# Kernel optimization log

Measured on AMD Instinct MI355X. Metric: run time of the kernel, lower is better.

The kernel has to match this reference:

```python
import jax, jax.numpy as jnp
import numpy as np

B, NE, NMAX = 256, 90, 270
ZE = PE = GE = PPS = 32
NPROPS = 20
FP, SGE, LATH = 256, 64, 128
PIN = FP + SGE + LATH  # 448 = pred_inp_size = conv input (add_to_node)
C1, C2, H = 448, 256, 3
P1 = P2 = 512
EPS = 1e-5

PNAMES = ['sg_emb_table','lat_W1','lat_b1','lat_bn1_g','lat_bn1_b','lat_bn1_m','lat_bn1_v',
          'lat_W2','lat_b2','lat_bn2_g','lat_bn2_b','lat_bn2_m','lat_bn2_v',
          'z_emb_table','period_table','group_table','props','W_props','b_props','W_phys','b_phys',
          'gat1_W','gat1_as','gat1_ad','gat1_b','gat2_W','gat2_as','gat2_ad','gat2_b',
          'pW1','pb1','pbn1_g','pbn1_b','pbn1_m','pbn1_v',
          'pW2','pb2','pbn2_g','pbn2_b','pbn2_m','pbn2_v','pW3','pb3']

def _bn(x, g, b, m, v):
    return (x - m) * g / jnp.sqrt(v + EPS) + b

def _lrelu(x, s=0.2):
    return jnp.where(x >= 0, x, s * x)

def _gat(x, adj, W, a_s, a_d, bias):
    # PyG DenseGATConv: concat=False (mean over heads), dropout=0, negative_slope=0.2
    Bn, N, _ = x.shape
    h = (x @ W).reshape(Bn, N, H, -1)                      # [B,N,H,C]
    asrc = (h * a_s).sum(-1)                               # [B,N,H]
    adst = (h * a_d).sum(-1)
    alpha = asrc[:, None, :, :] + adst[:, :, None, :]      # [B,i,j,H]
    alpha = _lrelu(alpha, 0.2)
    adj_sl = jnp.maximum(adj, jnp.eye(N, dtype=adj.dtype))  # add self loops
    alpha = jnp.where(adj_sl[..., None] > 0, alpha, -jnp.inf)
    alpha = jax.nn.softmax(alpha, axis=2)                  # softmax over sources j
    out = jnp.einsum('bijh,bjhc->bihc', alpha, h)
    return out.mean(2) + bias                              # [B,N,C]

def _forward(comp, sg, lat, period_idx, group_idx, p):
    sg_x = p['sg_emb_table'][sg[:, 0]]                     # [B,SGE]
    # lattice MLP: (Linear -> BN -> LeakyReLU(True)==identity) x2
    h = _bn(lat @ p['lat_W1'] + p['lat_b1'], p['lat_bn1_g'], p['lat_bn1_b'], p['lat_bn1_m'], p['lat_bn1_v'])
    lat_x = _bn(h @ p['lat_W2'] + p['lat_b2'], p['lat_bn2_g'], p['lat_bn2_b'], p['lat_bn2_m'], p['lat_bn2_v'])
    # ragged -> dense batch: expand composition counts into dense node-type grid
    n_atoms = comp.sum(1)                                  # [B]
    cum = jnp.cumsum(comp, axis=1)                         # [B,NE]
    t = jnp.arange(NMAX)
    z = jax.vmap(lambda c: jnp.searchsorted(c, t, side='right'))(cum)  # [B,NMAX]
    mask = t[None, :] < n_atoms[:, None]                   # [B,NMAX] valid nodes
    z = jnp.where(mask, z, 0)
    # PhysEmbedding: z/period/group embeddings + projected properties -> final proj
    phys = jnp.concatenate([
        p['z_emb_table'][z],
        p['period_table'][period_idx[z]],
        p['group_table'][group_idx[z]],
        p['props'][z] @ p['W_props'] + p['b_props'],
    ], axis=-1)
    phys = phys @ p['W_phys'] + p['b_phys']                # [B,NMAX,FP]
    # add_to_node: cat graph-level lat/sg embeddings onto every node, then zero-pad
    node = jnp.concatenate([
        phys,
        jnp.broadcast_to(lat_x[:, None, :], (lat_x.shape[0], NMAX, LATH)),
        jnp.broadcast_to(sg_x[:, None, :], (sg_x.shape[0], NMAX, SGE)),
    ], axis=-1)
    node = node * mask[..., None].astype(node.dtype)       # to_dense_batch zero padding
    # per-graph dense block adjacency, zero diagonal (fill_diagonal_(0))
    adj = (mask[:, :, None] & mask[:, None, :]).astype(node.dtype)
    adj = adj * (1.0 - jnp.eye(NMAX, dtype=node.dtype))
    # GNNBlock: act = LeakyReLU(True) == identity (negative_slope=1)
    x1 = _gat(node, adj, p['gat1_W'], p['gat1_as'], p['gat1_ad'], p['gat1_b'])
    x2 = _gat(x1, adj, p['gat2_W'], p['gat2_as'], p['gat2_ad'], p['gat2_b'])
    comp_x = x2.sum(1)                                     # sum over ALL NMAX slots (incl. padding, as torch does)
    feat = jnp.concatenate([comp_x, sg_x, lat_x], axis=-1) # [B,PIN]
    # prediction head (eval: dropout off, BN running stats)
    h = _lrelu(_bn(feat @ p['pW1'] + p['pb1'], p['pbn1_g'], p['pbn1_b'], p['pbn1_m'], p['pbn1_v']))
    h = _lrelu(_bn(h @ p['pW2'] + p['pb2'], p['pbn2_g'], p['pbn2_b'], p['pbn2_m'], p['pbn2_v']))
    return h @ p['pW3'] + p['pb3']                         # [B,1]

def setup_inputs():
    key = jax.random.key(0)
    ks = iter(jax.random.split(key, 64))
    def nrm(shape, s=0.05):
        return jax.random.normal(next(ks), shape, dtype=jnp.float32) * s
    comp = jax.random.randint(next(ks), (B, NE), 0, 4, dtype=jnp.int32)
    comp = comp.at[0].set(3)  # graph 0 has exactly NMAX atoms -> data N_max == NMAX
    sg = jax.random.randint(next(ks), (B, 1), 0, 230)
    lat = jax.random.uniform(next(ks), (B, 6), dtype=jnp.float32)
    period_idx = jax.random.randint(next(ks), (NE,), 0, 8)
    group_idx = jax.random.randint(next(ks), (NE,), 0, 19)
    inp = dict(comp=comp, sg=sg, lat=lat, period_idx=period_idx, group_idx=group_idx)
    inp.update(
        sg_emb_table=nrm((230, SGE)),
        lat_W1=nrm((6, LATH)), lat_b1=nrm((LATH,)),
        lat_bn1_g=jnp.ones(LATH), lat_bn1_b=jnp.zeros(LATH), lat_bn1_m=jnp.zeros(LATH), lat_bn1_v=jnp.ones(LATH),
        lat_W2=nrm((LATH, LATH)), lat_b2=nrm((LATH,)),
        lat_bn2_g=jnp.ones(LATH), lat_bn2_b=jnp.zeros(LATH), lat_bn2_m=jnp.zeros(LATH), lat_bn2_v=jnp.ones(LATH),
        z_emb_table=nrm((NE, ZE)), period_table=nrm((8, PE)), group_table=nrm((19, GE)),
        props=nrm((NE, NPROPS), 0.1), W_props=nrm((NPROPS, PPS)), b_props=nrm((PPS,)),
        W_phys=nrm((ZE + PE + GE + PPS, FP)), b_phys=nrm((FP,)),
        gat1_W=nrm((PIN, H * C1)), gat1_as=nrm((H, C1)), gat1_ad=nrm((H, C1)), gat1_b=nrm((C1,)),
        gat2_W=nrm((C1, H * C2)), gat2_as=nrm((H, C2)), gat2_ad=nrm((H, C2)), gat2_b=nrm((C2,)),
        pW1=nrm((PIN, P1)), pb1=nrm((P1,)),
        pbn1_g=jnp.ones(P1), pbn1_b=jnp.zeros(P1), pbn1_m=jnp.zeros(P1), pbn1_v=jnp.ones(P1),
        pW2=nrm((P1, P2)), pb2=nrm((P2,)),
        pbn2_g=jnp.ones(P2), pbn2_b=jnp.zeros(P2), pbn2_m=jnp.zeros(P2), pbn2_v=jnp.ones(P2),
        pW3=nrm((P2, 1)), pb3=nrm((1,)),
    )
    return inp

def reference(comp, sg, lat, period_idx, group_idx,
              sg_emb_table, lat_W1, lat_b1, lat_bn1_g, lat_bn1_b, lat_bn1_m, lat_bn1_v,
              lat_W2, lat_b2, lat_bn2_g, lat_bn2_b, lat_bn2_m, lat_bn2_v,
              z_emb_table, period_table, group_table, props, W_props, b_props, W_phys, b_phys,
              gat1_W, gat1_as, gat1_ad, gat1_b, gat2_W, gat2_as, gat2_ad, gat2_b,
              pW1, pb1, pbn1_g, pbn1_b, pbn1_m, pbn1_v,
              pW2, pb2, pbn2_g, pbn2_b, pbn2_m, pbn2_v, pW3, pb3):
    vals = (sg_emb_table, lat_W1, lat_b1, lat_bn1_g, lat_bn1_b, lat_bn1_m, lat_bn1_v,
            lat_W2, lat_b2, lat_bn2_g, lat_bn2_b, lat_bn2_m, lat_bn2_v,
            z_emb_table, period_table, group_table, props, W_props, b_props, W_phys, b_phys,
            gat1_W, gat1_as, gat1_ad, gat1_b, gat2_W, gat2_as, gat2_ad, gat2_b,
            pW1, pb1, pbn1_g, pbn1_b, pbn1_m, pbn1_v,
            pW2, pb2, pbn2_g, pbn2_b, pbn2_m, pbn2_v, pW3, pb3)
    p = dict(zip(PNAMES, vals))
    return _forward(comp, sg, lat, period_idx, group_idx, p)
```

## Files before the change

### kernel.cpp

```cpp
#include <hip/hip_runtime.h>
#include <math.h>

#define BB 256
#define NEL 90
#define NMAX 270
#define C1 448
#define C2 256
#define PIN 448
#define LATH 128
#define SGE 64
#define P1 512
#define EPSB 1e-5f

typedef short shortx8 __attribute__((ext_vector_type(8)));
typedef float floatx4 __attribute__((ext_vector_type(4)));

__device__ __forceinline__ float bf2f(unsigned short u) {
  return __uint_as_float(((unsigned)u) << 16);
}
__device__ __forceinline__ unsigned short f2bf(float f) {
  unsigned x = __float_as_uint(f);
  unsigned r = (x + 0x7fffu + ((x >> 16) & 1u)) >> 16;
  return (unsigned short)r;
}

#define NB_PREP  BB
#define NB_SCAN  1
#define NB_PHYS  NEL
#define NB_WP1   (14 * 42)
#define NB_WP2   (14 * 24)
#define NB_FOLD  112
#define NB_PAD   64
#define SETUP_GRID (NB_PREP + NB_SCAN + NB_PHYS + NB_WP1 + NB_WP2 + 2 * NB_FOLD + NB_PAD)

__global__ __launch_bounds__(256) void k_setup(
    const int* __restrict__ comp, const int* __restrict__ sg, const float* __restrict__ lat,
    const float* __restrict__ sg_emb,
    const float* __restrict__ lW1, const float* __restrict__ lb1,
    const float* __restrict__ lg1, const float* __restrict__ lbe1,
    const float* __restrict__ lm1, const float* __restrict__ lv1,
    const float* __restrict__ lW2, const float* __restrict__ lb2,
    const float* __restrict__ lg2, const float* __restrict__ lbe2,
    const float* __restrict__ lm2, const float* __restrict__ lv2,
    const int* __restrict__ period_idx, const int* __restrict__ group_idx,
    const float* __restrict__ z_emb, const float* __restrict__ period_t,
    const float* __restrict__ group_t, const float* __restrict__ props,
    const float* __restrict__ Wp, const float* __restrict__ bp,
    const float* __restrict__ Wphys, const float* __restrict__ bphys,
    const float* __restrict__ gat1_W, const float* __restrict__ gat1_as,
    const float* __restrict__ gat1_ad, const float* __restrict__ gat1_b,
    const float* __restrict__ gat2_W, const float* __restrict__ gat2_as,
    const float* __restrict__ gat2_ad, const float* __restrict__ gat2_b,
    float* __restrict__ sgx, float* __restrict__ latx, int* __restrict__ z,
    int* __restrict__ natoms, int* __restrict__ off, int* __restrict__ aoff,
    float* __restrict__ zerobuf, float* __restrict__ physpe,
    unsigned short* __restrict__ wt1, unsigned short* __restrict__ wt2,
    float* __restrict__ wsv1, float* __restrict__ wdv1,
    float* __restrict__ wsv2, float* __restrict__ wdv2, float* __restrict__ pad2) {
  int r = blockIdx.x;
  int tid = threadIdx.x;
  int wv = tid >> 6, lane = tid & 63;

  if (r < NB_PREP) {
    int b = r;
    __shared__ int cum[NEL];
    __shared__ float hbuf[LATH];
    __shared__ float latl[6];
    if (tid == 0) {
      int s = 0;
      for (int e = 0; e < NEL; ++e) { s += comp[b * NEL + e]; cum[e] = s; }
    }
    if (tid < 6) latl[tid] = lat[b * 6 + tid];
    __syncthreads();
    int n = cum[NEL - 1];
    for (int t = tid; t < NMAX; t += 256) {
      int zz = -1;
      if (t < n) {
        for (int e = 0; e < NEL; ++e) { if (cum[e] > t) { zz = e; break; } }
      }
      z[b * NMAX + t] = zz;
    }
    if (tid < SGE) sgx[b * SGE + tid] = sg_emb[sg[b] * SGE + tid];
    if (tid < LATH) {
      float acc = lb1[tid];
      for (int k = 0; k < 6; ++k) acc += latl[k] * lW1[k * LATH + tid];
      acc = (acc - lm1[tid]) * lg1[tid] * rsqrtf(lv1[tid] + EPSB) + lbe1[tid];
      hbuf[tid] = acc;
    }
    __syncthreads();
    if (tid < LATH) {
      float acc = lb2[tid];
      for (int k = 0; k < LATH; ++k) acc += hbuf[k] * lW2[k * LATH + tid];
      acc = (acc - lm2[tid]) * lg2[tid] * rsqrtf(lv2[tid] + EPSB) + lbe2[tid];
      latx[b * LATH + tid] = acc;
    }
    return;
  }
  r -= NB_PREP;
  if (r < NB_SCAN) {
    __shared__ int sh[BB];
    zerobuf[tid] = 0.f;
    int v0 = 0;
    for (int e = 0; e < NEL; ++e) v0 += comp[tid * NEL + e];
    natoms[tid] = v0;
    sh[tid] = v0;
    for (int d = 1; d < BB; d <<= 1) {
      __syncthreads();
      int v = (tid >= d) ? sh[tid - d] : 0;
      __syncthreads();
      sh[tid] += v;
    }
    __syncthreads();
    off[tid] = sh[tid] - v0;
    __syncthreads();
    int sz = 3 * ((((v0 + 15) >> 4) << 4)) * ((((v0 + 31) >> 5) << 5));
    sh[tid] = sz;
    for (int d = 1; d < BB; d <<= 1) {
      __syncthreads();
      int v = (tid >= d) ? sh[tid - d] : 0;
      __syncthreads();
      sh[tid] += v;
    }
    __syncthreads();
    aoff[tid] = sh[tid] - sz;
    return;
  }
  r -= NB_SCAN;
  if (r < NB_PHYS) {
    int e = r;
    __shared__ float ph[128];
    if (tid < 32) ph[tid] = z_emb[e * 32 + tid];
    else if (tid < 64) ph[tid] = period_t[period_idx[e] * 32 + tid - 32];
    else if (tid < 96) ph[tid] = group_t[group_idx[e] * 32 + tid - 64];
    else if (tid < 128) {
      int j = tid - 96;
      float acc = bp[j];
      for (int k = 0; k < 20; ++k) acc += props[e * 20 + k] * Wp[k * 32 + j];
      ph[tid] = acc;
    }
    __syncthreads();
    float acc = bphys[tid];
    for (int k = 0; k < 128; ++k) acc += ph[k] * Wphys[k * 256 + tid];
    physpe[e * 256 + tid] = acc;
    return;
  }
  r -= NB_PHYS;
  if (r < NB_WP1 + NB_WP2) {
    const float* W;
    unsigned short* Wt;
    int NC3, bx, by;
    if (r < NB_WP1) { W = gat1_W; Wt = wt1; NC3 = 3 * C1; bx = r % 14; by = r / 14; }
    else { int r2 = r - NB_WP1; W = gat2_W; Wt = wt2; NC3 = 3 * C2; bx = r2 % 14; by = r2 / 14; }
    int k0 = bx << 5, c0 = by << 5;
    __shared__ float ts[32][33];
    int e4 = tid << 2;
    int kk = e4 >> 5, cc = e4 & 31;
    float4 v = *(const float4*)(W + (size_t)(k0 + kk) * NC3 + c0 + cc);
    ts[kk][cc] = v.x; ts[kk][cc + 1] = v.y; ts[kk][cc + 2] = v.z; ts[kk][cc + 3] = v.w;
    __syncthreads();
    int c2 = tid & 31, kg = tid >> 5;
    ushort4 u;
    u.x = f2bf(ts[kg * 4 + 0][c2]); u.y = f2bf(ts[kg * 4 + 1][c2]);
    u.z = f2bf(ts[kg * 4 + 2][c2]); u.w = f2bf(ts[kg * 4 + 3][c2]);
    *(ushort4*)(Wt + (size_t)(c0 + c2) * 448 + k0 + (kg << 2)) = u;
    return;
  }
  r -= NB_WP1 + NB_WP2;
  if (r < 2 * NB_FOLD) {
    const float* W; const float* as_; const float* ad_;
    float* wsv; float* wdv; int NC3, C, kb;
    if (r < NB_FOLD) { W = gat1_W; as_ = gat1_as; ad_ = gat1_ad; wsv = wsv1; wdv = wdv1; NC3 = 3 * C1; C = C1; kb = r << 2; }
    else { int r2 = r - NB_FOLD; W = gat2_W; as_ = gat2_as; ad_ = gat2_ad; wsv = wsv2; wdv = wdv2; NC3 = 3 * C2; C = C2; kb = r2 << 2; }
    int k = kb + wv;
    for (int h = 0; h < 3; ++h) {
      float ss = 0.f, sd = 0.f;
      for (int c = lane; c < C; c += 64) {
        float wvv = W[(size_t)k * NC3 + h * C + c];
        ss += wvv * as_[h * C + c];
        sd += wvv * ad_[h * C + c];
      }
      for (int o = 32; o > 0; o >>= 1) { ss += __shfl_xor(ss, o); sd += __shfl_xor(sd, o); }
      if (lane == 0) { wsv[k * 3 + h] = ss; wdv[k * 3 + h] = sd; }
    }
    return;
  }
  r -= 2 * NB_FOLD;
  {
    int c = (r << 2) + wv;
    float s = 0.f;
    for (int k = lane; k < C1; k += 64) {
      const float* wr = gat2_W + (size_t)k * (3 * C2) + c;
      s += gat1_b[k] * (wr[0] + wr[C2] + wr[2 * C2]);
    }
    for (int o = 32; o > 0; o >>= 1) s += __shfl_xor(s, o);
    if (lane == 0) pad2[c] = s * (1.f / 3.f) + gat2_b[c];
  }
}

__global__ __launch_bounds__(256) void k_nodep(
    const int* __restrict__ z, const int* __restrict__ off, const int* __restrict__ natoms,
    const float* __restrict__ physpe, const float* __restrict__ latx,
    const float* __restrict__ sgx, unsigned short* __restrict__ x0) {
  int b = blockIdx.x;
  int n = natoms[b], ob = off[b];
  int tid = threadIdx.x;
  __shared__ int zl[NMAX];
  for (int t = tid; t < n; t += 256) zl[t] = z[b * NMAX + t];
  __syncthreads();
  int items = n * 56;
  for (int e = tid; e < items; e += 256) {
    int t = e / 56, c8 = (e - t * 56) << 3;
    int zt = zl[t];
    float v[8];
    if (c8 < 256) {
      float4 a = *(const float4*)(physpe + zt * 256 + c8);
      float4 c = *(const float4*)(physpe + zt * 256 + c8 + 4);
      v[0] = a.x; v[1] = a.y; v[2] = a.z; v[3] = a.w;
      v[4] = c.x; v[5] = c.y; v[6] = c.z; v[7] = c.w;
    } else if (c8 < 384) {
      float4 a = *(const float4*)(latx + b * LATH + c8 - 256);
      float4 c = *(const float4*)(latx + b * LATH + c8 - 252);
      v[0] = a.x; v[1] = a.y; v[2] = a.z; v[3] = a.w;
      v[4] = c.x; v[5] = c.y; v[6] = c.z; v[7] = c.w;
    } else {
      float4 a = *(const float4*)(sgx + b * SGE + c8 - 384);
      float4 c = *(const float4*)(sgx + b * SGE + c8 - 380);
      v[0] = a.x; v[1] = a.y; v[2] = a.z; v[3] = a.w;
      v[4] = c.x; v[5] = c.y; v[6] = c.z; v[7] = c.w;
    }
    unsigned short u[8];
    #pragma unroll
    for (int i = 0; i < 8; ++i) u[i] = f2bf(v[i]);
    *(uint4*)(x0 + (size_t)(ob + t) * PIN + c8) = *(uint4*)u;
  }
}

__global__ __launch_bounds__(256) void k_av2(
    const unsigned short* __restrict__ x, const float* __restrict__ wsv,
    const float* __restrict__ wdv, const int* __restrict__ off,
    const int* __restrict__ natoms, float* __restrict__ asrc,
    float* __restrict__ adst, int K) {
  __shared__ float sw[C1 * 3], dw[C1 * 3];
  int tid = threadIdx.x;
  for (int e = tid; e < K * 3; e += 256) { sw[e] = wsv[e]; dw[e] = wdv[e]; }
  __syncthreads();
  int total = off[BB - 1] + natoms[BB - 1];
  int wv = tid >> 6, lane = tid & 63;
  int nk8 = K >> 3;
  int stride = gridDim.x << 2;
  for (int row = (blockIdx.x << 2) + wv; row < total; row += stride) {
    float s0 = 0.f, s1 = 0.f, s2 = 0.f, d0 = 0.f, d1 = 0.f, d2 = 0.f;
    if (lane < nk8) {
      uint4 raw = *(const uint4*)(x + (size_t)row * K + (lane << 3));
      unsigned short us[8];
      *(uint4*)us = raw;
      #pragma unroll
      for (int u = 0; u < 8; ++u) {
        float xv = bf2f(us[u]);
        int kb = ((lane << 3) + u) * 3;
        s0 += xv * sw[kb + 0]; s1 += xv * sw[kb + 1]; s2 += xv * sw[kb + 2];
        d0 += xv * dw[kb + 0]; d1 += xv * dw[kb + 1]; d2 += xv * dw[kb + 2];
      }
    }
    #pragma unroll
    for (int o = 32; o > 0; o >>= 1) {
      s0 += __shfl_xor(s0, o); s1 += __shfl_xor(s1, o); s2 += __shfl_xor(s2, o);
      d0 += __shfl_xor(d0, o); d1 += __shfl_xor(d1, o); d2 += __shfl_xor(d2, o);
    }
    if (lane == 0) {
      asrc[row * 3 + 0] = s0; asrc[row * 3 + 1] = s1; asrc[row * 3 + 2] = s2;
      adst[row * 3 + 0] = d0; adst[row * 3 + 1] = d1; adst[row * 3 + 2] = d2;
    }
  }
}

#define MTMAX 17
__global__ __launch_bounds__(256) void k_alpha(
    const float* __restrict__ asrc, const float* __restrict__ adst,
    const int* __restrict__ off, const int* __restrict__ natoms,
    const int* __restrict__ aoff, unsigned short* __restrict__ alpha) {
  int bid = blockIdx.x;
  int b = bid & (BB - 1);
  int hm = bid >> 8;
  int h = hm % 3;
  int mt = hm / 3;
  int n = natoms[b];
  if (n == 0) return;
  int mtn = (n + 15) >> 4;
  if (mt >= mtn) return;
  int ktn = (n + 31) >> 5;
  int rext = mtn << 4, kext = ktn << 5;
  int ob = off[b];
  size_t ab = (size_t)aoff[b] + (size_t)h * rext * kext;
  int tid = threadIdx.x;
  int wv = tid >> 6, lane = tid & 63;
  __shared__ float asl[288];
  for (int j = tid; j < kext; j += 256)
    asl[j] = (j < n) ? asrc[(ob + j) * 3 + h] : 0.f;
  __syncthreads();
  #pragma unroll
  for (int r = 0; r < 4; ++r) {
    int i = (mt << 4) + (wv << 2) + r;
    unsigned short* rowp = alpha + ab + (size_t)i * kext;
    if (i >= n) {
      for (int j = lane; j < kext; j += 64) rowp[j] = 0;
      continue;
    }
    float ad = adst[(ob + i) * 3 + h];
    float m = -1e30f;
    for (int j = lane; j < n; j += 64) {
      float sc = asl[j] + ad;
      sc = fmaxf(sc, 0.2f * sc);
      m = fmaxf(m, sc);
    }
    for (int o = 32; o > 0; o >>= 1) m = fmaxf(m, __shfl_xor(m, o));
    float s = 0.f;
    for (int j = lane; j < n; j += 64) {
      float sc = asl[j] + ad;
      sc = fmaxf(sc, 0.2f * sc);
      s += __expf(sc - m);
    }
    for (int o = 32; o > 0; o >>= 1) s += __shfl_xor(s, o);
    float rs = 1.f / s;
    for (int j = lane; j < kext; j += 64) {
      float v = 0.f;
      if (j < n) {
        float sc = asl[j] + ad;
        sc = fmaxf(sc, 0.2f * sc);
        v = __expf(sc - m) * rs;
      }
      rowp[j] = f2bf(v);
    }
  }
}

#define MTW 5

__global__ __launch_bounds__(256, 2) void k_fused_mfma(
    const unsigned short* __restrict__ xin, const unsigned short* __restrict__ Wt,
    const unsigned short* __restrict__ alpha, const int* __restrict__ aoff,
    const int* __restrict__ off, const int* __restrict__ natoms,
    const float* __restrict__ bias, const float* __restrict__ zerobuf,
    unsigned short* __restrict__ xout, int K, int C, int NC) {
  int bid = blockIdx.x;
  int xg = bid & 7;
  int g = bid >> 3;
  int cblk = g % NC;
  int b = xg + ((g / NC) << 3);
  int c0 = cblk << 6;
  int n = natoms[b];
  if (n == 0) return;
  int ob = off[b];
  size_t ab = (size_t)aoff[b];
  int tid = threadIdx.x;
  int wv = tid >> 6;
  int lane = tid & 63;
  int m16 = lane & 15;
  int q = lane >> 4;

  int mtn = (n + 15) >> 4;
  int jmax = mtn << 4;
  int ktn = (n + 31) >> 5;
  int kext = ktn << 5;
  size_t hstride = (size_t)jmax * kext;

  __shared__ unsigned short tt[36 * 512];

  const unsigned short* xsrc[MTW];
  #pragma unroll
  for (int t_i = 0; t_i < MTW; ++t_i) {
    int mt = wv + (t_i << 2);
    int j = (mt << 4) + m16;
    xsrc[t_i] = (j < n) ? (xin + (size_t)(ob + j) * 448 + (q << 3))
                        : (const unsigned short*)zerobuf;
  }

  floatx4 acc[MTW][4];
  #pragma unroll
  for (int i = 0; i < MTW; ++i)
    #pragma unroll
    for (int nt = 0; nt < 4; ++nt) acc[i][nt] = (floatx4)0.f;

  for (int h = 0; h < 3; ++h) {
    floatx4 tac[MTW][4];
    #pragma unroll
    for (int i = 0; i < MTW; ++i)
      #pragma unroll
      for (int nt = 0; nt < 4; ++nt) tac[i][nt] = (floatx4)0.f;

    const unsigned short* wbase = Wt + (size_t)(h * C + c0 + m16) * 448 + (q << 3);

    #pragma unroll 2
    for (int k0 = 0; k0 < 448; k0 += 32) {
      shortx8 bfr[4];
      #pragma unroll
      for (int nt = 0; nt < 4; ++nt)
        bfr[nt] = *(const shortx8*)(wbase + (size_t)(nt << 4) * 448 + k0);
      #pragma unroll
      for (int t_i = 0; t_i < MTW; ++t_i) {
        int mt = wv + (t_i << 2);
        if (mt < mtn) {
          shortx8 a = *(const shortx8*)(xsrc[t_i] + k0);
          #pragma unroll
          for (int nt = 0; nt < 4; ++nt)
            tac[t_i][nt] = __builtin_amdgcn_mfma_f32_16x16x32_bf16(a, bfr[nt], tac[t_i][nt], 0, 0, 0);
        }
      }
    }

    #pragma unroll
    for (int t_i = 0; t_i < MTW; ++t_i) {
      int mt = wv + (t_i << 2);
      if (mt < mtn) {
        int jbase = (mt << 4) + (q << 2);
        #pragma unroll
        for (int nt = 0; nt < 4; ++nt) {
          floatx4 d = tac[t_i][nt];
          ushort4 u;
          u.x = f2bf(d.x); u.y = f2bf(d.y); u.z = f2bf(d.z); u.w = f2bf(d.w);
          int c = (nt << 4) + m16;
          *(ushort4*)(tt + ((jbase >> 3) << 9) + (c << 3) + (jbase & 7)) = u;
        }
      }
    }
    for (int e = tid; e < ((kext - jmax) << 6); e += 256) {
      int j = jmax + (e >> 6), c = e & 63;
      tt[((j >> 3) << 9) + (c << 3) + (j & 7)] = 0;
    }
    __syncthreads();
    const unsigned short* ap = alpha + ab + (size_t)h * hstride;
    for (int k0p = 0; k0p < kext; k0p += 32) {
      shortx8 tb[4];
      #pragma unroll
      for (int nt = 0; nt < 4; ++nt)
        tb[nt] = *(const shortx8*)(tt + (((k0p >> 3) + q) << 9) + (((nt << 4) + m16) << 3));
      #pragma unroll
      for (int t_i = 0; t_i < MTW; ++t_i) {
        int mt = wv + (t_i << 2);
        if (mt < mtn) {
          shortx8 af = *(const shortx8*)(ap + (size_t)((mt << 4) + m16) * kext + k0p + (q << 3));
          #pragma unroll
          for (int nt = 0; nt < 4; ++nt)
            acc[t_i][nt] = __builtin_amdgcn_mfma_f32_16x16x32_bf16(af, tb[nt], acc[t_i][nt], 0, 0, 0);
        }
      }
    }
    __syncthreads();
  }
  float bq[4];
  #pragma unroll
  for (int nt = 0; nt < 4; ++nt) bq[nt] = bias[c0 + (nt << 4) + m16];
  const float inv3 = 1.f / 3.f;
  #pragma unroll
  for (int t_i = 0; t_i < MTW; ++t_i) {
    int mt = wv + (t_i << 2);
    if (mt < mtn) {
      #pragma unroll
      for (int nt = 0; nt < 4; ++nt) {
        floatx4 d = acc[t_i][nt];
        int cidx = c0 + (nt << 4) + m16;
        #pragma unroll
        for (int r = 0; r < 4; ++r) {
          int i = (mt << 4) + (q << 2) + r;
          if (i < n) xout[(size_t)(ob + i) * C + cidx] = f2bf(d[r] * inv3 + bq[nt]);
        }
      }
    }
  }
}

__global__ __launch_bounds__(512) void k_feat_head(
    const unsigned short* __restrict__ x2, const float* __restrict__ pad2,
    const int* __restrict__ off, const int* __restrict__ natoms,
    const float* __restrict__ sgx, const float* __restrict__ latx,
    const float* __restrict__ W1, const float* __restrict__ b1,
    const float* __restrict__ g1, const float* __restrict__ be1,
    const float* __restrict__ m1, const float* __restrict__ v1,
    const float* __restrict__ W2, const float* __restrict__ b2,
    const float* __restrict__ g2, const float* __restrict__ be2,
    const float* __restrict__ m2, const float* __restrict__ v2,
    const float* __restrict__ W3, const float* __restrict__ b3,
    float* __restrict__ out) {
  int b = blockIdx.x, tid = threadIdx.x;
  int wv8 = tid >> 6, lane = tid & 63;
  int n = natoms[b], ob = off[b];
  __shared__ float part[8][256];
  __shared__ float f[PIN];
  __shared__ float h1[P1];
  __shared__ float h2[P1];
  __shared__ float red[512];
  float a0 = 0.f, a1 = 0.f, a2 = 0.f, a3 = 0.f;
  for (int r = wv8; r < n; r += 8) {
    uint2 raw = *(const uint2*)(x2 + (size_t)(ob + r) * C2 + (lane << 2));
    unsigned short us[4];
    *(uint2*)us = raw;
    a0 += bf2f(us[0]); a1 += bf2f(us[1]); a2 += bf2f(us[2]); a3 += bf2f(us[3]);
  }
  {
    float4 p = make_float4(a0, a1, a2, a3);
    *(float4*)&part[wv8][lane << 2] = p;
  }
  __syncthreads();
  if (tid < 256) {
    float s = 0.f;
    #pragma unroll
    for (int w = 0; w < 8; ++w) s += part[w][tid];
    f[tid] = s + (float)(NMAX - n) * pad2[tid];
  } else if (tid < 320) {
    f[tid] = sgx[b * SGE + (tid - 256)];
  } else if (tid < 448) {
    f[tid] = latx[b * LATH + (tid - 320)];
  }
  __syncthreads();
  {
    int o = tid;
    float acc = b1[o];
    for (int k = 0; k < PIN; ++k) acc += f[k] * W1[k * P1 + o];
    acc = (acc - m1[o]) * g1[o] * rsqrtf(v1[o] + EPSB) + be1[o];
    h1[o] = acc >= 0.f ? acc : 0.2f * acc;
  }
  __syncthreads();
  {
    int o = tid;
    float acc = b2[o];
    for (int k = 0; k < P1; ++k) acc += h1[k] * W2[k * P1 + o];
    acc = (acc - m2[o]) * g2[o] * rsqrtf(v2[o] + EPSB) + be2[o];
    h2[o] = acc >= 0.f ? acc : 0.2f * acc;
  }
  __syncthreads();
  red[tid] = h2[tid] * W3[tid];
  __syncthreads();
  for (int s = 256; s > 0; s >>= 1) {
    if (tid < s) red[tid] += red[tid + s];
    __syncthreads();
  }
  if (tid == 0) out[b] = red[0] + b3[0];
}

extern "C" void kernel_launch(void* const* d_in, const int* in_sizes, int n_in,
                              void* d_out, int out_size, void* d_ws, size_t ws_size,
                              hipStream_t stream) {
  const int*   comp       = (const int*)d_in[0];
  const int*   sg         = (const int*)d_in[1];
  const float* lat        = (const float*)d_in[2];
  const int*   period_idx = (const int*)d_in[3];
  const int*   group_idx  = (const int*)d_in[4];
  const float* sg_emb     = (const float*)d_in[5];
  const float* lat_W1     = (const float*)d_in[6];
  const float* lat_b1     = (const float*)d_in[7];
  const float* lat_bn1_g  = (const float*)d_in[8];
  const float* lat_bn1_b  = (const float*)d_in[9];
  const float* lat_bn1_m  = (const float*)d_in[10];
  const float* lat_bn1_v  = (const float*)d_in[11];
  const float* lat_W2     = (const float*)d_in[12];
  const float* lat_b2     = (const float*)d_in[13];
  const float* lat_bn2_g  = (const float*)d_in[14];
  const float* lat_bn2_b  = (const float*)d_in[15];
  const float* lat_bn2_m  = (const float*)d_in[16];
  const float* lat_bn2_v  = (const float*)d_in[17];
  const float* z_emb      = (const float*)d_in[18];
  const float* period_t   = (const float*)d_in[19];
  const float* group_t    = (const float*)d_in[20];
  const float* props      = (const float*)d_in[21];
  const float* W_props    = (const float*)d_in[22];
  const float* b_props    = (const float*)d_in[23];
  const float* W_phys     = (const float*)d_in[24];
  const float* b_phys     = (const float*)d_in[25];
  const float* gat1_W     = (const float*)d_in[26];
  const float* gat1_as    = (const float*)d_in[27];
  const float* gat1_ad    = (const float*)d_in[28];
  const float* gat1_b     = (const float*)d_in[29];
  const float* gat2_W     = (const float*)d_in[30];
  const float* gat2_as    = (const float*)d_in[31];
  const float* gat2_ad    = (const float*)d_in[32];
  const float* gat2_b     = (const float*)d_in[33];
  const float* pW1        = (const float*)d_in[34];
  const float* pb1        = (const float*)d_in[35];
  const float* pbn1_g     = (const float*)d_in[36];
  const float* pbn1_b     = (const float*)d_in[37];
  const float* pbn1_m     = (const float*)d_in[38];
  const float* pbn1_v     = (const float*)d_in[39];
  const float* pW2        = (const float*)d_in[40];
  const float* pb2        = (const float*)d_in[41];
  const float* pbn2_g     = (const float*)d_in[42];
  const float* pbn2_b     = (const float*)d_in[43];
  const float* pbn2_m     = (const float*)d_in[44];
  const float* pbn2_v     = (const float*)d_in[45];
  const float* pW3        = (const float*)d_in[46];
  const float* pb3        = (const float*)d_in[47];

  float* ws = (float*)d_ws;
  const size_t o_sgx  = 0;
  const size_t o_latx = o_sgx  + (size_t)BB * SGE;
  const size_t o_nat  = o_latx + (size_t)BB * LATH;
  const size_t o_off  = o_nat  + BB;
  const size_t o_aoff = o_off  + BB;
  const size_t o_z    = o_aoff + BB;
  const size_t o_phys = o_z    + (size_t)BB * NMAX;
  const size_t o_wsv1 = o_phys + (size_t)NEL * 256;
  const size_t o_wdv1 = o_wsv1 + (size_t)C1 * 3;
  const size_t o_wsv2 = o_wdv1 + (size_t)C1 * 3;
  const size_t o_wdv2 = o_wsv2 + (size_t)C1 * 3;
  const size_t o_asrc = o_wdv2 + (size_t)C1 * 3;
  const size_t o_adst = o_asrc + (size_t)BB * NMAX * 3;
  const size_t o_pad2 = o_adst + (size_t)BB * NMAX * 3;
  const size_t o_zero = o_pad2 + 256;
  const size_t o_wt1  = o_zero + 256;
  const size_t o_wt2  = o_wt1  + (size_t)(3 * C1) * PIN / 2;
  const size_t o_x0   = o_wt2  + (size_t)(3 * C2) * C1 / 2;
  const size_t o_x1   = o_x0   + (size_t)BB * NMAX * PIN / 2;
  const size_t o_alph = o_x1   + (size_t)BB * NMAX * PIN / 2;

  float* sgx    = ws + o_sgx;
  float* latx   = ws + o_latx;
  int*   natoms = (int*)(ws + o_nat);
  int*   off    = (int*)(ws + o_off);
  int*   aoff   = (int*)(ws + o_aoff);
  int*   z      = (int*)(ws + o_z);
  float* physpe = ws + o_phys;
  float* wsv1   = ws + o_wsv1;
  float* wdv1   = ws + o_wdv1;
  float* wsv2   = ws + o_wsv2;
  float* wdv2   = ws + o_wdv2;
  float* asrc   = ws + o_asrc;
  float* adst   = ws + o_adst;
  float* pad2   = ws + o_pad2;
  float* zerobuf = ws + o_zero;
  unsigned short* wt1   = (unsigned short*)(ws + o_wt1);
  unsigned short* wt2   = (unsigned short*)(ws + o_wt2);
  unsigned short* x0    = (unsigned short*)(ws + o_x0);
  unsigned short* x1    = (unsigned short*)(ws + o_x1);
  unsigned short* x2    = x0;
  unsigned short* alpha = (unsigned short*)(ws + o_alph);

  const int ALG = BB * 3 * MTMAX;

  k_setup<<<SETUP_GRID, 256, 0, stream>>>(
      comp, sg, lat, sg_emb,
      lat_W1, lat_b1, lat_bn1_g, lat_bn1_b, lat_bn1_m, lat_bn1_v,
      lat_W2, lat_b2, lat_bn2_g, lat_bn2_b, lat_bn2_m, lat_bn2_v,
      period_idx, group_idx, z_emb, period_t, group_t, props,
      W_props, b_props, W_phys, b_phys,
      gat1_W, gat1_as, gat1_ad, gat1_b,
      gat2_W, gat2_as, gat2_ad, gat2_b,
      sgx, latx, z, natoms, off, aoff, zerobuf, physpe,
      wt1, wt2, wsv1, wdv1, wsv2, wdv2, pad2);

  k_nodep<<<BB, 256, 0, stream>>>(z, off, natoms, physpe, latx, sgx, x0);

  k_av2<<<1024, 256, 0, stream>>>(x0, wsv1, wdv1, off, natoms, asrc, adst, PIN);
  k_alpha<<<ALG, 256, 0, stream>>>(asrc, adst, off, natoms, aoff, alpha);
  k_fused_mfma<<<(C1 / 64) * BB, 256, 0, stream>>>(x0, wt1, alpha, aoff,
      off, natoms, gat1_b, zerobuf, x1, PIN, C1, C1 / 64);

  k_av2<<<1024, 256, 0, stream>>>(x1, wsv2, wdv2, off, natoms, asrc, adst, C1);
  k_alpha<<<ALG, 256, 0, stream>>>(asrc, adst, off, natoms, aoff, alpha);
  k_fused_mfma<<<(C2 / 64) * BB, 256, 0, stream>>>(x1, wt2, alpha, aoff,
      off, natoms, gat2_b, zerobuf, x2, C1, C2, C2 / 64);

  k_feat_head<<<BB, 512, 0, stream>>>(x2, pad2, off, natoms, sgx, latx,
      pW1, pb1, pbn1_g, pbn1_b, pbn1_m, pbn1_v,
      pW2, pb2, pbn2_g, pbn2_b, pbn2_m, pbn2_v,
      pW3, pb3, (float*)d_out);
}
```

Baseline: 878.0 us.

## Stage weight tiles into LDS via global_load_lds with XOR swizzle

Instead of every wave loading the weight B-fragments straight from global memory, the kernel stages a 32-row by 448-column weight slice into shared memory (reusing the tt buffer) with asynchronous global_load_lds. Reads use an XOR swizzle to avoid bank conflicts. The goal is to stop four waves from redundantly fetching the same weights and to cut global load latency in the MFMA inner loop. The cost is two extra block barriers per half-slice per head and no overlap between the staging load and compute, since the loads are not double-buffered.

New measurement: 832.6 us. 1.05x faster.

```diff
diff --git a/kernel.cpp b/kernel.cpp
--- a/kernel.cpp
+++ b/kernel.cpp
@@ -22,6 +22,11 @@
   unsigned x = __float_as_uint(f);
   unsigned r = (x + 0x7fffu + ((x >> 16) & 1u)) >> 16;
   return (unsigned short)r;
+}
+__device__ __forceinline__ void gld16(const void* g, void* l) {
+  __builtin_amdgcn_global_load_lds(
+      (const __attribute__((address_space(1))) unsigned int*)g,
+      (__attribute__((address_space(3))) unsigned int*)l, 16, 0, 0);
 }
 
 #define NB_PREP  BB
@@ -335,6 +340,8 @@
 }
 
 #define MTW 5
+#define WROWS 32
+#define WCH 56
 
 __global__ __launch_bounds__(256, 2) void k_fused_mfma(
     const unsigned short* __restrict__ xin, const unsigned short* __restrict__ Wt,
@@ -365,6 +372,16 @@
   size_t hstride = (size_t)jmax * kext;
 
   __shared__ unsigned short tt[36 * 512];
+  unsigned short* wlds = tt;
+
+  int swz16[7];
+  #pragma unroll
+  for (int i = 0; i < 7; ++i) {
+    int d16 = (i << 8) + tid;
+    int row = d16 / WCH;
+    int ch = d16 - row * WCH;
+    swz16[i] = row * WCH + (ch ^ (row & 7));
+  }
 
   const unsigned short* xsrc[MTW];
   #pragma unroll
@@ -388,24 +405,35 @@
       #pragma unroll
       for (int nt = 0; nt < 4; ++nt) tac[i][nt] = (floatx4)0.f;
 
-    const unsigned short* wbase = Wt + (size_t)(h * C + c0 + m16) * 448 + (q << 3);
-
-    #pragma unroll 2
-    for (int k0 = 0; k0 < 448; k0 += 32) {
-      shortx8 bfr[4];
+    #pragma unroll
+    for (int r = 0; r < 2; ++r) {
+      const unsigned short* wsl = Wt + (size_t)(h * C + c0 + r * WROWS) * 448;
       #pragma unroll
-      for (int nt = 0; nt < 4; ++nt)
-        bfr[nt] = *(const shortx8*)(wbase + (size_t)(nt << 4) * 448 + k0);
-      #pragma unroll
-      for (int t_i = 0; t_i < MTW; ++t_i) {
-        int mt = wv + (t_i << 2);
-        if (mt < mtn) {
-          shortx8 a = *(const shortx8*)(xsrc[t_i] + k0);
-          #pragma unroll
-          for (int nt = 0; nt < 4; ++nt)
-            tac[t_i][nt] = __builtin_amdgcn_mfma_f32_16x16x32_bf16(a, bfr[nt], tac[t_i][nt], 0, 0, 0);
+      for (int i = 0; i < 7; ++i)
+        gld16(wsl + ((size_t)swz16[i] << 3), wlds + ((((i << 8) + (wv << 6))) << 3));
+      __syncthreads();
+      #pragma unroll 2
+      for (int k0 = 0; k0 < 448; k0 += 32) {
+        int kq = (k0 >> 3) + q;
+        shortx8 bfr[2];
+        #pragma unroll
+        for (int nt2 = 0; nt2 < 2; ++nt2) {
+          int row = (nt2 << 4) + m16;
+          bfr[nt2] = *(const shortx8*)(wlds + row * 448 + ((kq ^ (row & 7)) << 3));
         }
-      }
+        #pragma unroll
+        for (int t_i = 0; t_i < MTW; ++t_i) {
+          int mt = wv + (t_i << 2);
+          if (mt < mtn) {
+            shortx8 a = *(const shortx8*)(xsrc[t_i] + k0);
+            tac[t_i][(r << 1) + 0] = __builtin_amdgcn_mfma_f32_16x16x32_bf16(
+                a, bfr[0], tac[t_i][(r << 1) + 0], 0, 0, 0);
+            tac[t_i][(r << 1) + 1] = __builtin_amdgcn_mfma_f32_16x16x32_bf16(
+                a, bfr[1], tac[t_i][(r << 1) + 1], 0, 0, 0);
+          }
+        }
+      }
+      __syncthreads();
     }
 
     #pragma unroll
```

## Split fused GAT kernel into global X·W GEMM and per-graph aggregation

Applied to the files above, without the earlier changes.

Replaces the per-graph fused kernel, which recomputed X·W for each graph and head inside a block, with a batch-wide tiled bf16 MFMA GEMM. The GEMM uses 128x64 tiles, double-buffered global_load_lds and a swizzled LDS layout, and writes transposed XW to a scratch buffer. A second kernel then does the alpha·XW aggregation per graph from that buffer. Node offsets are padded to multiples of 32 with zeroed pad rows so the aggregation can read contiguous K-tiles. The work is chunked across column blocks to keep the scratch buffer small. This improves weight reuse and MFMA utilisation, but adds a global-memory round trip and more kernel launches.

Measured after the change: 1.008 ms. +14.8%, slower.

```diff
diff --git a/kernel.cpp b/kernel.cpp
--- a/kernel.cpp
+++ b/kernel.cpp
@@ -12,6 +12,9 @@
 #define P1 512
 #define EPSB 1e-5f
 
+#define XROWCAP 44032
+#define GJT (XROWCAP / 128)
+
 typedef short shortx8 __attribute__((ext_vector_type(8)));
 typedef float floatx4 __attribute__((ext_vector_type(4)));
 
@@ -22,6 +25,11 @@
   unsigned x = __float_as_uint(f);
   unsigned r = (x + 0x7fffu + ((x >> 16) & 1u)) >> 16;
   return (unsigned short)r;
+}
+__device__ __forceinline__ void gld16(const void* g, void* l) {
+  __builtin_amdgcn_global_load_lds(
+      (const __attribute__((address_space(1))) unsigned int*)g,
+      (__attribute__((address_space(3))) unsigned int*)l, 16, 0, 0);
 }
 
 #define NB_PREP  BB
@@ -53,6 +61,7 @@
     const float* __restrict__ gat2_ad, const float* __restrict__ gat2_b,
     float* __restrict__ sgx, float* __restrict__ latx, int* __restrict__ z,
     int* __restrict__ natoms, int* __restrict__ off, int* __restrict__ aoff,
+    int* __restrict__ meta,
     float* __restrict__ zerobuf, float* __restrict__ physpe,
     unsigned short* __restrict__ wt1, unsigned short* __restrict__ wt2,
     float* __restrict__ wsv1, float* __restrict__ wdv1,
@@ -103,7 +112,8 @@
     int v0 = 0;
     for (int e = 0; e < NEL; ++e) v0 += comp[tid * NEL + e];
     natoms[tid] = v0;
-    sh[tid] = v0;
+    int kx = ((v0 + 31) >> 5) << 5;
+    sh[tid] = kx;
     for (int d = 1; d < BB; d <<= 1) {
       __syncthreads();
       int v = (tid >= d) ? sh[tid - d] : 0;
@@ -111,7 +121,8 @@
       sh[tid] += v;
     }
     __syncthreads();
-    off[tid] = sh[tid] - v0;
+    off[tid] = sh[tid] - kx;
+    if (tid == BB - 1) meta[0] = sh[tid];
     __syncthreads();
     int sz = 3 * ((((v0 + 15) >> 4) << 4)) * ((((v0 + 31) >> 5) << 5));
     sh[tid] = sz;
@@ -232,6 +243,13 @@
     #pragma unroll
     for (int i = 0; i < 8; ++i) u[i] = f2bf(v[i]);
     *(uint4*)(x0 + (size_t)(ob + t) * PIN + c8) = *(uint4*)u;
+  }
+  int kext = ((n + 31) >> 5) << 5;
+  int pitems = (kext - n) * 56;
+  for (int e = tid; e < pitems; e += 256) {
+    int rr = e / 56, c8 = (e - rr * 56) << 3;
+    uint4 z4; z4.x = z4.y = z4.z = z4.w = 0u;
+    *(uint4*)(x0 + (size_t)(ob + n + rr) * PIN + c8) = z4;
   }
 }
 
@@ -334,118 +352,145 @@
   }
 }
 
+__global__ __launch_bounds__(256, 4) void k_gemm(
+    const unsigned short* __restrict__ X, const unsigned short* __restrict__ W,
+    const int* __restrict__ meta, const float* __restrict__ zerobuf,
+    unsigned short* __restrict__ xwT, int C, int cb0, int ncb) {
+  int total = meta[0];
+  int NBT = 3 * ncb;
+  int mb = blockIdx.x / NBT;
+  int m0 = mb << 7;
+  if (m0 >= total) return;
+  int nb = blockIdx.x - mb * NBT;
+  int h = nb / ncb;
+  int i = nb - h * ncb;
+  int colbase = h * C + ((cb0 + i) << 6);
+  int bandbase = nb << 6;
+  int tid = threadIdx.x;
+  int wv = tid >> 6, lane = tid & 63;
+  int m16 = lane & 15, q = lane >> 4;
+
+  __shared__ unsigned short As[2][128 * 32];
+  __shared__ unsigned short Bs[2][64 * 32];
+
+  int l4 = lane >> 2, ci = lane & 3;
+  int ra0 = (wv << 4) + l4;
+  int ra1 = ra0 + 64;
+  int rb  = (wv << 4) + l4;
+  const unsigned short* asrc0 = (m0 + ra0 < total)
+      ? (X + (size_t)(m0 + ra0) * 448 + ((ci ^ (ra0 & 3)) << 3))
+      : (const unsigned short*)zerobuf;
+  const unsigned short* asrc1 = (m0 + ra1 < total)
+      ? (X + (size_t)(m0 + ra1) * 448 + ((ci ^ (ra1 & 3)) << 3))
+      : (const unsigned short*)zerobuf;
+  const unsigned short* bsrc = W + (size_t)(colbase + rb) * 448 + ((ci ^ (rb & 3)) << 3);
+
+  floatx4 acc[2][4];
+  #pragma unroll
+  for (int ti = 0; ti < 2; ++ti)
+    #pragma unroll
+    for (int nt = 0; nt < 4; ++nt) acc[ti][nt] = (floatx4)0.f;
+
+  gld16(asrc0, &As[0][wv << 9]);
+  gld16(asrc1, &As[0][2048 + (wv << 9)]);
+  gld16(bsrc, &Bs[0][wv << 9]);
+  __syncthreads();
+
+  #pragma unroll 2
+  for (int s = 0; s < 14; ++s) {
+    int cur = s & 1;
+    if (s < 13) {
+      int k1 = (s + 1) << 5;
+      int nxt = cur ^ 1;
+      gld16(asrc0 + k1, &As[nxt][wv << 9]);
+      gld16(asrc1 + k1, &As[nxt][2048 + (wv << 9)]);
+      gld16(bsrc + k1, &Bs[nxt][wv << 9]);
+    }
+    const unsigned short* Ab = As[cur];
+    const unsigned short* Bb = Bs[cur];
+    shortx8 bfr[4];
+    #pragma unroll
+    for (int nt = 0; nt < 4; ++nt) {
+      int rr = (nt << 4) + m16;
+      bfr[nt] = *(const shortx8*)(Bb + rr * 32 + ((q ^ (rr & 3)) << 3));
+    }
+    #pragma unroll
+    for (int ti = 0; ti < 2; ++ti) {
+      int ra = ((((wv << 1) + ti) << 4) + m16);
+      shortx8 a = *(const shortx8*)(Ab + ra * 32 + ((q ^ (ra & 3)) << 3));
+      #pragma unroll
+      for (int nt = 0; nt < 4; ++nt)
+        acc[ti][nt] = __builtin_amdgcn_mfma_f32_16x16x32_bf16(a, bfr[nt], acc[ti][nt], 0, 0, 0);
+    }
+    __syncthreads();
+  }
+
+  #pragma unroll
+  for (int ti = 0; ti < 2; ++ti) {
+    int j0 = m0 + (((wv << 1) + ti) << 4) + (q << 2);
+    if (j0 < total) {
+      #pragma unroll
+      for (int nt = 0; nt < 4; ++nt) {
+        int cr = bandbase + (nt << 4) + m16;
+        floatx4 d = acc[ti][nt];
+        ushort4 u;
+        u.x = f2bf(d[0]); u.y = f2bf(d[1]); u.z = f2bf(d[2]); u.w = f2bf(d[3]);
+        *(ushort4*)(xwT + (size_t)cr * total + j0) = u;
+      }
+    }
+  }
+}
+
 #define MTW 5
-
-__global__ __launch_bounds__(256, 2) void k_fused_mfma(
-    const unsigned short* __restrict__ xin, const unsigned short* __restrict__ Wt,
-    const unsigned short* __restrict__ alpha, const int* __restrict__ aoff,
-    const int* __restrict__ off, const int* __restrict__ natoms,
-    const float* __restrict__ bias, const float* __restrict__ zerobuf,
-    unsigned short* __restrict__ xout, int K, int C, int NC) {
-  int bid = blockIdx.x;
-  int xg = bid & 7;
-  int g = bid >> 3;
-  int cblk = g % NC;
-  int b = xg + ((g / NC) << 3);
-  int c0 = cblk << 6;
+__global__ __launch_bounds__(256, 3) void k_phaseB(
+    const unsigned short* __restrict__ xwT, const unsigned short* __restrict__ alpha,
+    const int* __restrict__ aoff, const int* __restrict__ off,
+    const int* __restrict__ natoms, const int* __restrict__ meta,
+    const float* __restrict__ bias, unsigned short* __restrict__ xout,
+    int C, int cb0, int ncb) {
+  int pitch = meta[0];
+  int i = blockIdx.x / BB;
+  int b = blockIdx.x - i * BB;
+  int c0 = (cb0 + i) << 6;
   int n = natoms[b];
   if (n == 0) return;
   int ob = off[b];
   size_t ab = (size_t)aoff[b];
   int tid = threadIdx.x;
-  int wv = tid >> 6;
-  int lane = tid & 63;
-  int m16 = lane & 15;
-  int q = lane >> 4;
-
+  int wv = tid >> 6, lane = tid & 63;
+  int m16 = lane & 15, q = lane >> 4;
   int mtn = (n + 15) >> 4;
   int jmax = mtn << 4;
   int ktn = (n + 31) >> 5;
   int kext = ktn << 5;
   size_t hstride = (size_t)jmax * kext;
 
-  __shared__ unsigned short tt[36 * 512];
-
-  const unsigned short* xsrc[MTW];
-  #pragma unroll
-  for (int t_i = 0; t_i < MTW; ++t_i) {
-    int mt = wv + (t_i << 2);
-    int j = (mt << 4) + m16;
-    xsrc[t_i] = (j < n) ? (xin + (size_t)(ob + j) * 448 + (q << 3))
-                        : (const unsigned short*)zerobuf;
-  }
-
   floatx4 acc[MTW][4];
   #pragma unroll
-  for (int i = 0; i < MTW; ++i)
+  for (int t_i = 0; t_i < MTW; ++t_i)
     #pragma unroll
-    for (int nt = 0; nt < 4; ++nt) acc[i][nt] = (floatx4)0.f;
+    for (int nt = 0; nt < 4; ++nt) acc[t_i][nt] = (floatx4)0.f;
 
   for (int h = 0; h < 3; ++h) {
-    floatx4 tac[MTW][4];
-    #pragma unroll
-    for (int i = 0; i < MTW; ++i)
-      #pragma unroll
-      for (int nt = 0; nt < 4; ++nt) tac[i][nt] = (floatx4)0.f;
-
-    const unsigned short* wbase = Wt + (size_t)(h * C + c0 + m16) * 448 + (q << 3);
-
+    const unsigned short* ap = alpha + ab + (size_t)h * hstride + (q << 3);
+    const unsigned short* xb = xwT + (size_t)(((h * ncb + i) << 6) + m16) * pitch + ob + (q << 3);
     #pragma unroll 2
-    for (int k0 = 0; k0 < 448; k0 += 32) {
-      shortx8 bfr[4];
+    for (int k0p = 0; k0p < kext; k0p += 32) {
+      shortx8 tb[4];
       #pragma unroll
       for (int nt = 0; nt < 4; ++nt)
-        bfr[nt] = *(const shortx8*)(wbase + (size_t)(nt << 4) * 448 + k0);
+        tb[nt] = *(const shortx8*)(xb + (size_t)(nt << 4) * pitch + k0p);
       #pragma unroll
       for (int t_i = 0; t_i < MTW; ++t_i) {
         int mt = wv + (t_i << 2);
         if (mt < mtn) {
-          shortx8 a = *(const shortx8*)(xsrc[t_i] + k0);
-          #pragma unroll
-          for (int nt = 0; nt < 4; ++nt)
-            tac[t_i][nt] = __builtin_amdgcn_mfma_f32_16x16x32_bf16(a, bfr[nt], tac[t_i][nt], 0, 0, 0);
-        }
-      }
-    }
-
-    #pragma unroll
-    for (int t_i = 0; t_i < MTW; ++t_i) {
-      int mt = wv + (t_i << 2);
-      if (mt < mtn) {
-        int jbase = (mt << 4) + (q << 2);
-        #pragma unroll
-        for (int nt = 0; nt < 4; ++nt) {
-          floatx4 d = tac[t_i][nt];
-          ushort4 u;
-          u.x = f2bf(d.x); u.y = f2bf(d.y); u.z = f2bf(d.z); u.w = f2bf(d.w);
-          int c = (nt << 4) + m16;
-          *(ushort4*)(tt + ((jbase >> 3) << 9) + (c << 3) + (jbase & 7)) = u;
-        }
-      }
-    }
-    for (int e = tid; e < ((kext - jmax) << 6); e += 256) {
-      int j = jmax + (e >> 6), c = e & 63;
-      tt[((j >> 3) << 9) + (c << 3) + (j & 7)] = 0;
-    }
-    __syncthreads();
-    const unsigned short* ap = alpha + ab + (size_t)h * hstride;
-    for (int k0p = 0; k0p < kext; k0p += 32) {
-      shortx8 tb[4];
-      #pragma unroll
-      for (int nt = 0; nt < 4; ++nt)
-        tb[nt] = *(const shortx8*)(tt + (((k0p >> 3) + q) << 9) + (((nt << 4) + m16) << 3));
-      #pragma unroll
-      for (int t_i = 0; t_i < MTW; ++t_i) {
-        int mt = wv + (t_i << 2);
-        if (mt < mtn) {
-          shortx8 af = *(const shortx8*)(ap + (size_t)((mt << 4) + m16) * kext + k0p + (q << 3));
+          shortx8 af = *(const shortx8*)(ap + (size_t)((mt << 4) + m16) * kext + k0p);
           #pragma unroll
           for (int nt = 0; nt < 4; ++nt)
             acc[t_i][nt] = __builtin_amdgcn_mfma_f32_16x16x32_bf16(af, tb[nt], acc[t_i][nt], 0, 0, 0);
         }
       }
     }
-    __syncthreads();
   }
   float bq[4];
   #pragma unroll
@@ -461,11 +506,17 @@
         int cidx = c0 + (nt << 4) + m16;
         #pragma unroll
         for (int r = 0; r < 4; ++r) {
-          int i = (mt << 4) + (q << 2) + r;
-          if (i < n) xout[(size_t)(ob + i) * C + cidx] = f2bf(d[r] * inv3 + bq[nt]);
+          int ii = (mt << 4) + (q << 2) + r;
+          if (ii < n) xout[(size_t)(ob + ii) * C + cidx] = f2bf(d[r] * inv3 + bq[nt]);
         }
       }
     }
+  }
+  for (int e = tid; e < ((kext - n) << 4); e += 256) {
+    int row = n + (e >> 4);
+    int c = c0 + ((e & 15) << 2);
+    ushort4 z4; z4.x = z4.y = z4.z = z4.w = 0;
+    *(ushort4*)(xout + (size_t)(ob + row) * C + c) = z4;
   }
 }
 
@@ -595,7 +646,8 @@
   const size_t o_nat  = o_latx + (size_t)BB * LATH;
   const size_t o_off  = o_nat  + BB;
   const size_t o_aoff = o_off  + BB;
-  const size_t o_z    = o_aoff + BB;
+  const size_t o_meta = o_aoff + BB;
+  const size_t o_z    = o_meta + 64;
   const size_t o_phys = o_z    + (size_t)BB * NMAX;
   const size_t o_wsv1 = o_phys + (size_t)NEL * 256;
   const size_t o_wdv1 = o_wsv1 + (size_t)C1 * 3;
@@ -608,14 +660,16 @@
   const size_t o_wt1  = o_zero + 256;
   const size_t o_wt2  = o_wt1  + (size_t)(3 * C1) * PIN / 2;
   const size_t o_x0   = o_wt2  + (size_t)(3 * C2) * C1 / 2;
-  const size_t o_x1   = o_x0   + (size_t)BB * NMAX * PIN / 2;
-  const size_t o_alph = o_x1   + (size_t)BB * NMAX * PIN / 2;
+  const size_t o_x1   = o_x0   + (size_t)XROWCAP * PIN / 2;
+  const size_t o_alph = o_x1   + (size_t)XROWCAP * PIN / 2;
+  const size_t o_xwt  = o_alph + 9500000;
 
   float* sgx    = ws + o_sgx;
   float* latx   = ws + o_latx;
   int*   natoms = (int*)(ws + o_nat);
   int*   off    = (int*)(ws + o_off);
   int*   aoff   = (int*)(ws + o_aoff);
+  int*   meta   = (int*)(ws + o_meta);
   int*   z      = (int*)(ws + o_z);
   float* physpe = ws + o_phys;
   float* wsv1   = ws + o_wsv1;
@@ -631,6 +685,7 @@
   unsigned short* x0    = (unsigned short*)(ws + o_x0);
   unsigned short* x1    = (unsigned short*)(ws + o_x1);
   unsigned short* x2    = x0;
+  unsigned short* xwT   = (unsigned short*)(ws + o_xwt);
   unsigned short* alpha = (unsigned short*)(ws + o_alph);
 
   const int ALG = BB * 3 * MTMAX;
@@ -643,20 +698,32 @@
       W_props, b_props, W_phys, b_phys,
       gat1_W, gat1_as, gat1_ad, gat1_b,
       gat2_W, gat2_as, gat2_ad, gat2_b,
-      sgx, latx, z, natoms, off, aoff, zerobuf, physpe,
+      sgx, latx, z, natoms, off, aoff, meta, zerobuf, physpe,
       wt1, wt2, wsv1, wdv1, wsv2, wdv2, pad2);
 
   k_nodep<<<BB, 256, 0, stream>>>(z, off, natoms, physpe, latx, sgx, x0);
 
   k_av2<<<1024, 256, 0, stream>>>(x0, wsv1, wdv1, off, natoms, asrc, adst, PIN);
   k_alpha<<<ALG, 256, 0, stream>>>(asrc, adst, off, natoms, aoff, alpha);
-  k_fused_mfma<<<(C1 / 64) * BB, 256, 0, stream>>>(x0, wt1, alpha, aoff,
-      off, natoms, gat1_b, zerobuf, x1, PIN, C1, C1 / 64);
+  {
+    const int cbs[4] = {0, 2, 4, 6};
+    const int ncbs[4] = {2, 2, 2, 1};
+    for (int c = 0; c < 4; ++c) {
+      k_gemm<<<GJT * 3 * ncbs[c], 256, 0, stream>>>(x0, wt1, meta, zerobuf,
+          xwT, C1, cbs[c], ncbs[c]);
+      k_phaseB<<<ncbs[c] * BB, 256, 0, stream>>>(xwT, alpha, aoff, off, natoms,
+          meta, gat1_b, x1, C1, cbs[c], ncbs[c]);
+    }
+  }
 
   k_av2<<<1024, 256, 0, stream>>>(x1, wsv2, wdv2, off, natoms, asrc, adst, C1);
   k_alpha<<<ALG, 256, 0, stream>>>(asrc, adst, off, natoms, aoff, alpha);
-  k_fused_mfma<<<(C2 / 64) * BB, 256, 0, stream>>>(x1, wt2, alpha, aoff,
-      off, natoms, gat2_b, zerobuf, x2, C1, C2, C2 / 64);
+  for (int c = 0; c < 2; ++c) {
+    k_gemm<<<GJT * 6, 256, 0, stream>>>(x1, wt2, meta, zerobuf,
+        xwT, C2, c * 2, 2);
+    k_phaseB<<<2 * BB, 256, 0, stream>>>(xwT, alpha, aoff, off, natoms,
+        meta, gat2_b, x2, C2, c * 2, 2);
+  }
 
   k_feat_head<<<BB, 512, 0, stream>>>(x2, pad2, off, natoms, sgx, latx,
       pW1, pb1, pbn1_g, pbn1_b, pbn1_m, pbn1_v,
```
